# Kernel optimization log

Measured on AMD Instinct MI355X. Metric: run time of the kernel, lower is better.

The kernel has to match this reference:

```python
import jax, jax.numpy as jnp
import numpy as np

MASK_P = 0.15
MASK_LEN = 8
B, H, W, C = 64, 512, 256, 4


def setup_inputs() -> dict:
    key = jax.random.key(0)
    k1, k2, k3, k4, k5 = jax.random.split(key, 5)
    x = jax.random.normal(k1, (B, H, W, C), dtype=jnp.float32)
    time_rand = jax.random.uniform(k2, (B, MASK_LEN, W, C), dtype=jnp.float32)
    freq_rand = jax.random.uniform(k3, (B, H, MASK_LEN, C), dtype=jnp.float32)
    time_starts = jax.random.randint(k4, (B,), 0, H - MASK_LEN + 1, dtype=jnp.int32)
    freq_starts = jax.random.randint(k5, (B,), 0, W - MASK_LEN + 1, dtype=jnp.int32)
    return {"x": x, "time_rand": time_rand, "freq_rand": freq_rand,
            "time_starts": time_starts, "freq_starts": freq_starts}


def _combined_mask(time_rand, freq_rand, time_starts, freq_starts, h, w):
    # Bernoulli masks from uniform draws (cast of comparison, like tf.cast(u < p))
    tmask = jnp.where(time_rand < MASK_P, 1.0, 0.0)   # [B, L, W, C]
    fmask = jnp.where(freq_rand < MASK_P, 1.0, 0.0)   # [B, H, L, C]

    # --- time masking: pad each sample's [L,W,C] strip to height h at start_i,
    # then (faithful to the original broadcast) take product over the batch.
    rel_h = jnp.arange(h)[None, :] - time_starts[:, None]          # [B, H]
    valid_h = (rel_h >= 0) & (rel_h < MASK_LEN)                    # [B, H]
    idx_h = jnp.clip(rel_h, 0, MASK_LEN - 1)[:, :, None, None]    # [B, H, 1, 1]
    padded_t = jnp.take_along_axis(tmask, idx_h, axis=1)           # [B, H, W, C]
    padded_t = jnp.where(valid_h[:, :, None, None], padded_t, 0.0)
    mask_t = jnp.prod(1.0 - padded_t, axis=0)                      # [H, W, C]

    # --- freq masking, same pattern along the width axis.
    rel_w = jnp.arange(w)[None, :] - freq_starts[:, None]          # [B, W]
    valid_w = (rel_w >= 0) & (rel_w < MASK_LEN)                    # [B, W]
    idx_w = jnp.clip(rel_w, 0, MASK_LEN - 1)[:, None, :, None]    # [B, 1, W, 1]
    padded_f = jnp.take_along_axis(fmask, idx_w, axis=2)           # [B, H, W, C]
    padded_f = jnp.where(valid_w[:, None, :, None], padded_f, 0.0)
    mask_f = jnp.prod(1.0 - padded_f, axis=0)                      # [H, W, C]

    return mask_t * mask_f                                         # [H, W, C]


def reference(x, time_rand, freq_rand, time_starts, freq_starts):
    b, h, w, c = x.shape
    mask = _combined_mask(time_rand, freq_rand, time_starts, freq_starts, h, w)
    return x * mask[None]  # same mask broadcast over batch, as in the original
```

## Files before the change

### kernel.cpp

```cpp
#include <hip/hip_runtime.h>

constexpr int B_ = 64, H_ = 512, W_ = 256, C_ = 4, L_ = 8;
constexpr int WC   = W_ * C_;
constexpr int HWC  = H_ * WC;
constexpr int ROWS = 2;
constexpr int BCH  = 8;

__global__ __launch_bounds__(256)
void mask_apply_f32(const float* __restrict__ x,
                    const float* __restrict__ trand,
                    const float* __restrict__ frand,
                    const int* __restrict__ tstart,
                    const int* __restrict__ fstart,
                    float* __restrict__ out) {
    __shared__ int flagw[ROWS * WC / 4];
    __shared__ int ts_s[B_], fs_s[B_];
    unsigned char* flags = (unsigned char*)flagw;

    const int t  = threadIdx.x;
    const int h0 = blockIdx.x * ROWS;
    const int b0 = blockIdx.y * BCH;

    flagw[2 * t] = 0; flagw[2 * t + 1] = 0;
    if (t < B_) { ts_s[t] = tstart[t]; fs_s[t] = fstart[t]; }
    __syncthreads();

    for (int b = 0; b < B_; ++b) {
        int ts = ts_s[b];
#pragma unroll
        for (int r = 0; r < ROWS; ++r) {
            int l = h0 + r - ts;
            if ((unsigned)l < (unsigned)L_) {
                const float* row = trand + (b * L_ + l) * WC;
#pragma unroll
                for (int k = 0; k < 4; ++k) {
                    int i = t * 4 + k;
                    if (row[i] < 0.15f) flags[r * WC + i] = 1;
                }
            }
        }
    }

    {
        int bsub = t >> 5, lane = t & 31;
        int l = lane >> 2, c = lane & 3;
        for (int bb = 0; bb < B_; bb += 8) {
            int b  = bb + bsub;
            int fs = fs_s[b];
#pragma unroll
            for (int r = 0; r < ROWS; ++r) {
                float v = frand[(b * H_ + h0 + r) * (L_ * C_) + l * C_ + c];
                if (v < 0.15f) flags[r * WC + (fs + l) * C_ + c] = 1;
            }
        }
    }
    __syncthreads();

    const unsigned fw0 = (unsigned)flagw[t];
    const unsigned fw1 = (unsigned)flagw[256 + t];
    for (int bi = 0; bi < BCH; ++bi) {
        int base = (b0 + bi) * HWC + h0 * WC;
        float4 v0 = ((const float4*)(x + base))[t];
        float4 v1 = ((const float4*)(x + base + WC))[t];
        if (fw0) {
            if (fw0 & 0xffu)       v0.x = 0.f;
            if (fw0 & 0xff00u)     v0.y = 0.f;
            if (fw0 & 0xff0000u)   v0.z = 0.f;
            if (fw0 & 0xff000000u) v0.w = 0.f;
        }
        if (fw1) {
            if (fw1 & 0xffu)       v1.x = 0.f;
            if (fw1 & 0xff00u)     v1.y = 0.f;
            if (fw1 & 0xff0000u)   v1.z = 0.f;
            if (fw1 & 0xff000000u) v1.w = 0.f;
        }
        ((float4*)(out + base))[t]      = v0;
        ((float4*)(out + base + WC))[t] = v1;
    }
}

extern "C" void kernel_launch(void* const* d_in, const int* in_sizes, int n_in,
                              void* d_out, int out_size, void* d_ws, size_t ws_size,
                              hipStream_t stream) {
    const float* x  = (const float*)d_in[0];
    const float* tr = (const float*)d_in[1];
    const float* fr = (const float*)d_in[2];
    const int*   ts = (const int*)d_in[3];
    const int*   fs = (const int*)d_in[4];
    float* out = (float*)d_out;

    dim3 grid(H_ / ROWS, B_ / BCH);
    mask_apply_f32<<<grid, 256, 0, stream>>>(x, tr, fr, ts, fs, out);
}
```

Baseline: 264.8 us.

## Split mask construction from application using a workspace mask buffer

Adds a separate kernel that builds the full H×W×C float mask once per row, writing it to the workspace, followed by a simple streaming multiply kernel over x with 4 float4 loads per thread. The fused kernel, which rebuilt flags in every block (including scanning all batches per block), is kept only as a fallback when the workspace is too small. This removes redundant per-block mask construction. The cost is an extra kernel launch and an extra 2 MB mask read per batch, which is L2-resident.

```diff
diff --git a/kernel.cpp b/kernel.cpp
--- a/kernel.cpp
+++ b/kernel.cpp
@@ -1,30 +1,77 @@
 #include <hip/hip_runtime.h>
 
 constexpr int B_ = 64, H_ = 512, W_ = 256, C_ = 4, L_ = 8;
-constexpr int WC   = W_ * C_;
-constexpr int HWC  = H_ * WC;
-constexpr int ROWS = 2;
-constexpr int BCH  = 8;
+constexpr int WC    = W_ * C_;
+constexpr int HWC   = H_ * WC;
+constexpr int MWC4  = HWC / 4;
+constexpr long long N4 = 8388608LL;
 
 __global__ __launch_bounds__(256)
-void mask_apply_f32(const float* __restrict__ x,
-                    const float* __restrict__ trand,
-                    const float* __restrict__ frand,
-                    const int* __restrict__ tstart,
-                    const int* __restrict__ fstart,
-                    float* __restrict__ out) {
+void build_mask(const float* __restrict__ trand, const float* __restrict__ frand,
+                const int* __restrict__ tstart, const int* __restrict__ fstart,
+                float* __restrict__ mask) {
+    __shared__ int ts_s[B_], fs_s[B_];
+    const int t = threadIdx.x;
+    const int h = blockIdx.x;
+    if (t < B_) { ts_s[t] = tstart[t]; fs_s[t] = fstart[t]; }
+    __syncthreads();
+
+    float m0 = 1.f, m1 = 1.f, m2 = 1.f, m3 = 1.f;
+    for (int b = 0; b < B_; ++b) {
+        int lt = h - ts_s[b];
+        if ((unsigned)lt < (unsigned)L_) {
+            float4 v = *(const float4*)(trand + ((b * L_ + lt) * W_ + t) * C_);
+            if (v.x < 0.15f) m0 = 0.f;
+            if (v.y < 0.15f) m1 = 0.f;
+            if (v.z < 0.15f) m2 = 0.f;
+            if (v.w < 0.15f) m3 = 0.f;
+        }
+        int lw = t - fs_s[b];
+        if ((unsigned)lw < (unsigned)L_) {
+            float4 v = *(const float4*)(frand + ((b * H_ + h) * L_ + lw) * C_);
+            if (v.x < 0.15f) m0 = 0.f;
+            if (v.y < 0.15f) m1 = 0.f;
+            if (v.z < 0.15f) m2 = 0.f;
+            if (v.w < 0.15f) m3 = 0.f;
+        }
+    }
+    *(float4*)(mask + (h * W_ + t) * C_) = make_float4(m0, m1, m2, m3);
+}
+
+__global__ __launch_bounds__(256)
+void apply_mask(const float4* __restrict__ x4, const float4* __restrict__ m4,
+                float4* __restrict__ out4) {
+    const int base = blockIdx.x * 1024 + threadIdx.x;
+    float4 a0 = x4[base];
+    float4 a1 = x4[base + 256];
+    float4 a2 = x4[base + 512];
+    float4 a3 = x4[base + 768];
+    float4 b0 = m4[ base         & (MWC4 - 1)];
+    float4 b1 = m4[(base +  256) & (MWC4 - 1)];
+    float4 b2 = m4[(base +  512) & (MWC4 - 1)];
+    float4 b3 = m4[(base +  768) & (MWC4 - 1)];
+    a0.x *= b0.x; a0.y *= b0.y; a0.z *= b0.z; a0.w *= b0.w;
+    a1.x *= b1.x; a1.y *= b1.y; a1.z *= b1.z; a1.w *= b1.w;
+    a2.x *= b2.x; a2.y *= b2.y; a2.z *= b2.z; a2.w *= b2.w;
+    a3.x *= b3.x; a3.y *= b3.y; a3.z *= b3.z; a3.w *= b3.w;
+    out4[base]       = a0;
+    out4[base + 256] = a1;
+    out4[base + 512] = a2;
+    out4[base + 768] = a3;
+}
+
+constexpr int ROWS = 2, BCH = 8;
+__global__ __launch_bounds__(256)
+void mask_apply_fused(const float* __restrict__ x, const float* __restrict__ trand,
+                      const float* __restrict__ frand, const int* __restrict__ tstart,
+                      const int* __restrict__ fstart, float* __restrict__ out) {
     __shared__ int flagw[ROWS * WC / 4];
     __shared__ int ts_s[B_], fs_s[B_];
     unsigned char* flags = (unsigned char*)flagw;
-
-    const int t  = threadIdx.x;
-    const int h0 = blockIdx.x * ROWS;
-    const int b0 = blockIdx.y * BCH;
-
+    const int t = threadIdx.x, h0 = blockIdx.x * ROWS, b0 = blockIdx.y * BCH;
     flagw[2 * t] = 0; flagw[2 * t + 1] = 0;
     if (t < B_) { ts_s[t] = tstart[t]; fs_s[t] = fstart[t]; }
     __syncthreads();
-
     for (int b = 0; b < B_; ++b) {
         int ts = ts_s[b];
 #pragma unroll
@@ -33,47 +80,36 @@
             if ((unsigned)l < (unsigned)L_) {
                 const float* row = trand + (b * L_ + l) * WC;
 #pragma unroll
-                for (int k = 0; k < 4; ++k) {
-                    int i = t * 4 + k;
-                    if (row[i] < 0.15f) flags[r * WC + i] = 1;
-                }
+                for (int k = 0; k < 4; ++k)
+                    if (row[t * 4 + k] < 0.15f) flags[r * WC + t * 4 + k] = 1;
             }
         }
     }
-
     {
-        int bsub = t >> 5, lane = t & 31;
-        int l = lane >> 2, c = lane & 3;
+        int bsub = t >> 5, lane = t & 31, l = lane >> 2, c = lane & 3;
         for (int bb = 0; bb < B_; bb += 8) {
-            int b  = bb + bsub;
-            int fs = fs_s[b];
+            int b = bb + bsub, fs = fs_s[b];
 #pragma unroll
             for (int r = 0; r < ROWS; ++r) {
-                float v = frand[(b * H_ + h0 + r) * (L_ * C_) + l * C_ + c];
-                if (v < 0.15f) flags[r * WC + (fs + l) * C_ + c] = 1;
+                float vf = frand[(b * H_ + h0 + r) * (L_ * C_) + l * C_ + c];
+                if (vf < 0.15f) flags[r * WC + (fs + l) * C_ + c] = 1;
             }
         }
     }
     __syncthreads();
-
-    const unsigned fw0 = (unsigned)flagw[t];
-    const unsigned fw1 = (unsigned)flagw[256 + t];
+    const unsigned fw0 = (unsigned)flagw[t], fw1 = (unsigned)flagw[256 + t];
     for (int bi = 0; bi < BCH; ++bi) {
         int base = (b0 + bi) * HWC + h0 * WC;
         float4 v0 = ((const float4*)(x + base))[t];
         float4 v1 = ((const float4*)(x + base + WC))[t];
-        if (fw0) {
-            if (fw0 & 0xffu)       v0.x = 0.f;
-            if (fw0 & 0xff00u)     v0.y = 0.f;
-            if (fw0 & 0xff0000u)   v0.z = 0.f;
-            if (fw0 & 0xff000000u) v0.w = 0.f;
-        }
-        if (fw1) {
-            if (fw1 & 0xffu)       v1.x = 0.f;
-            if (fw1 & 0xff00u)     v1.y = 0.f;
-            if (fw1 & 0xff0000u)   v1.z = 0.f;
-            if (fw1 & 0xff000000u) v1.w = 0.f;
-        }
+        if (fw0 & 0xffu)       v0.x = 0.f;
+        if (fw0 & 0xff00u)     v0.y = 0.f;
+        if (fw0 & 0xff0000u)   v0.z = 0.f;
+        if (fw0 & 0xff000000u) v0.w = 0.f;
+        if (fw1 & 0xffu)       v1.x = 0.f;
+        if (fw1 & 0xff00u)     v1.y = 0.f;
+        if (fw1 & 0xff0000u)   v1.z = 0.f;
+        if (fw1 & 0xff000000u) v1.w = 0.f;
         ((float4*)(out + base))[t]      = v0;
         ((float4*)(out + base + WC))[t] = v1;
     }
@@ -89,6 +125,13 @@
     const int*   fs = (const int*)d_in[4];
     float* out = (float*)d_out;
 
-    dim3 grid(H_ / ROWS, B_ / BCH);
-    mask_apply_f32<<<grid, 256, 0, stream>>>(x, tr, fr, ts, fs, out);
+    if (ws_size >= (size_t)HWC * sizeof(float)) {
+        float* mask = (float*)d_ws;
+        build_mask<<<H_, 256, 0, stream>>>(tr, fr, ts, fs, mask);
+        apply_mask<<<(int)(N4 / 1024), 256, 0, stream>>>(
+            (const float4*)x, (const float4*)mask, (float4*)out);
+    } else {
+        dim3 grid(H_ / ROWS, B_ / BCH);
+        mask_apply_fused<<<grid, 256, 0, stream>>>(x, tr, fr, ts, fs, out);
+    }
 }
```

Measured after the change: 251.6 us. 5.0% less time.
